# Optimization experiments

Measured on AMD Instinct MI355X. Metric: run time of the kernel, lower is better.

Reference implementation:

```python
import jax, jax.numpy as jnp
import numpy as np

N = 8192        # nodes
E = 131072      # template edges (avg degree 16)
IN_DIM = 2
H = 128         # hidden_dim
Z = 128         # z_dim
MAX_DEPTH = 32
DEPTH_PERTURB = 2
NEG = -1e30


def setup_inputs() -> dict:
    key = jax.random.key(0)
    ks = jax.random.split(key, 24)
    s = 0.05
    # template node features: col0 = node type in {0,1,2}, col1 = placeholder
    types = jax.random.randint(ks[0], (N,), 0, 3)
    x = jnp.stack([types.astype(jnp.float32),
                   jax.random.normal(ks[1], (N,))], axis=1)
    edge_index = jax.random.randint(ks[2], (2, E), 0, N)
    node_depth = jnp.sort(jax.random.randint(ks[3], (N,), 0, MAX_DEPTH))
    z = jax.random.normal(ks[4], (Z,))
    return {
        "x": x, "z": z,
        "edge_index": edge_index, "node_depth": node_depth,
        # GCNConv 1 & 2 (PyG style: y = x @ W^T, symmetric-normalized agg, + bias)
        "conv1_w": jax.random.normal(ks[5], (H, IN_DIM)) * s,
        "conv1_b": jnp.zeros((H,)),
        "conv2_w": jax.random.normal(ks[6], (H, H)) * s,
        "conv2_b": jnp.zeros((H,)),
        # node_proj: Linear(H+Z,H) -> ReLU -> Linear(H,H)
        "np1_w": jax.random.normal(ks[7], (H, H + Z)) * s,
        "np1_b": jnp.zeros((H,)),
        "np2_w": jax.random.normal(ks[8], (H, H)) * s,
        "np2_b": jnp.zeros((H,)),
        # src/tgt projections (bias-free)
        "src_w": jax.random.normal(ks[9], (H, H)) * s,
        "tgt_w": jax.random.normal(ks[10], (H, H)) * s,
        # inv_mlp: Linear(2H+Z,H) -> ReLU -> Linear(H,1)
        "inv1_w": jax.random.normal(ks[11], (H, 2 * H + Z)) * s,
        "inv1_b": jnp.zeros((H,)),
        "inv2_w": jax.random.normal(ks[12], (1, H)) * s,
        "inv2_b": jnp.zeros((1,)),
    }


def _gcn_conv(x, src, dst, W, b, n):
    # PyG GCNConv with self loops: out_i = sum_j norm_ij * (x_j W^T) + b
    xw = x @ W.T                                             # [n, out]
    deg = jax.ops.segment_sum(jnp.ones(src.shape, xw.dtype), dst,
                              num_segments=n) + 1.0          # self-loop
    rsq = jax.lax.rsqrt(deg)
    msg = (rsq[src] * rsq[dst])[:, None] * xw[src]           # [E, out]
    agg = jax.ops.segment_sum(msg, dst, num_segments=n)
    agg = agg + xw / deg[:, None]                            # self-loop term
    return agg + b


def reference(x, z, edge_index, node_depth,
              conv1_w, conv1_b, conv2_w, conv2_b,
              np1_w, np1_b, np2_w, np2_b,
              src_w, tgt_w, inv1_w, inv1_b, inv2_w, inv2_b):
    n = x.shape[0]
    types = x[:, 0].astype(jnp.int32)
    src, dst = edge_index[0], edge_index[1]

    # --- GCN encode ---
    h = jax.nn.relu(_gcn_conv(x, src, dst, conv1_w, conv1_b, n))
    h = jax.nn.relu(_gcn_conv(h, src, dst, conv2_w, conv2_b, n))

    # --- node_proj with broadcast z ---
    hz = jnp.concatenate([h, jnp.broadcast_to(z[None, :], (n, Z))], axis=1)
    h = jax.nn.relu(hz @ np1_w.T + np1_b) @ np2_w.T + np2_b  # [n, H]

    # --- vectorized per-target candidate attention scores ---
    Ht = h @ tgt_w.T                                         # [n, H]
    Hs = h @ src_w.T                                         # [n, H]
    scores = Ht @ Hs.T                                       # [n, n]: S[v,u]
    depth = node_depth
    # candidate u valid for target v iff depth[u] <= depth[v]-1+perturb
    cand_mask = depth[None, :] <= (depth[:, None] - 1 + DEPTH_PERTURB)
    scores_m = jnp.where(cand_mask, scores, NEG)
    top_vals, top_idx = jax.lax.top_k(scores_m, 2)           # [n,2] each

    num_cand = cand_mask.sum(axis=1)
    target_valid = (depth >= 1) & (types != 0)
    # type==2 (AND) gets k=2 fanins, other non-PI types k=1
    valid = jnp.stack([target_valid & (num_cand >= 1),
                       target_valid & (types == 2) & (num_cand >= 2)], axis=1)

    # --- per-edge inversion-bit MLP (vectorized over [n, 2] chosen edges) ---
    h_u = h[top_idx]                                         # [n,2,H]
    h_v = jnp.broadcast_to(h[:, None, :], (n, 2, H))
    z_b = jnp.broadcast_to(z[None, None, :], (n, 2, Z))
    inv_in = jnp.concatenate([h_u, h_v, z_b], axis=-1)       # [n,2,2H+Z]
    inv_logit = (jax.nn.relu(inv_in @ inv1_w.T + inv1_b) @ inv2_w.T + inv2_b)[..., 0]
    inv_bit = (jax.nn.sigmoid(inv_logit) > 0.5).astype(jnp.int32)

    return top_vals, inv_logit, top_idx, inv_bit, valid
```

## Files before the change

### kernel.cpp

```cpp
#include <hip/hip_runtime.h>

#define NN 8192
#define EE 131072
#define HH 128
#define NEGV -1.0e30f
#define SEG 128
#define NSEG (NN / SEG)
#define VT 128

typedef __attribute__((ext_vector_type(8))) short bf16x8;
typedef __attribute__((ext_vector_type(4))) float f32x4;

__device__ __forceinline__ unsigned short f2bf(float f) {
    unsigned int u = __float_as_uint(f);
    unsigned int r = u + 0x7fffu + ((u >> 16) & 1u);
    return (unsigned short)(r >> 16);
}
__device__ __forceinline__ float bf2f(unsigned short b) {
    return __uint_as_float((unsigned int)b << 16);
}


__global__ __launch_bounds__(256) void k_deg(const int* __restrict__ dst, int* __restrict__ degi) {
    int t = blockIdx.x * 256 + threadIdx.x;
    if (t < EE) atomicAdd(&degi[dst[t]], 1);
}

__global__ __launch_bounds__(1024) void k_scan(const int* __restrict__ degi, int* __restrict__ rowptr,
                                               float* __restrict__ dinv, float* __restrict__ rsq) {
    __shared__ int ls[1024];
    int tid = threadIdx.x;
    int base = tid * 8;
    int loc[8]; int s = 0;
#pragma unroll
    for (int i = 0; i < 8; i++) {
        int dg = degi[base + i];
        loc[i] = s; s += dg;
        double d = (double)(dg + 1);
        dinv[base + i] = (float)(1.0 / d);
        rsq[base + i] = (float)(1.0 / sqrt(d));
    }
    ls[tid] = s; __syncthreads();
    int tot = s;
    for (int d = 1; d < 1024; d <<= 1) {
        int v = (tid >= d) ? ls[tid - d] : 0;
        __syncthreads();
        ls[tid] += v;
        __syncthreads();
    }
    int pre = ls[tid] - tot;
#pragma unroll
    for (int i = 0; i < 8; i++) rowptr[base + i] = pre + loc[i];
    if (tid == 1023) rowptr[NN] = pre + tot;
}

__global__ __launch_bounds__(256) void k_fill(const int* __restrict__ src, const int* __restrict__ dst,
                                              const int* __restrict__ rowptr, int* __restrict__ cursor,
                                              int* __restrict__ ecsr) {
    int t = blockIdx.x * 256 + threadIdx.x;
    if (t < EE) {
        int d = dst[t];
        int pos = atomicAdd(&cursor[d], 1);
        ecsr[rowptr[d] + pos] = src[t];
    }
}


__global__ __launch_bounds__(256) void k_gather1(const int* __restrict__ rowptr, const int* __restrict__ ecsr,
                                                 const float* __restrict__ rsq, const float* __restrict__ dinv,
                                                 const float* __restrict__ x, const float* __restrict__ w,
                                                 const float* __restrict__ bias, float* __restrict__ out) {
    int g = blockIdx.x * 256 + threadIdx.x;
    int d = g >> 6, lane = g & 63;
    if (d >= NN) return;
    float w0a = w[lane * 2], w1a = w[lane * 2 + 1];
    float w0b = w[(lane + 64) * 2], w1b = w[(lane + 64) * 2 + 1];
    int s0 = rowptr[d], s1 = rowptr[d + 1];
    float rd = rsq[d];
    float a0 = 0.f, a1 = 0.f;
    for (int sl = s0; sl < s1; sl++) {
        int s = ecsr[sl];
        float x0 = x[s * 2], x1 = x[s * 2 + 1];
        float f = rsq[s] * rd;
        a0 = fmaf(f, x0 * w0a + x1 * w1a, a0);
        a1 = fmaf(f, x0 * w0b + x1 * w1b, a1);
    }
    float x0d = x[d * 2], x1d = x[d * 2 + 1], di = dinv[d];
    a0 = fmaf(x0d * w0a + x1d * w1a, di, a0) + bias[lane];
    a1 = fmaf(x0d * w0b + x1d * w1b, di, a1) + bias[64 + lane];
    out[d * HH + lane] = fmaxf(a0, 0.f);
    out[d * HH + 64 + lane] = fmaxf(a1, 0.f);
}


__global__ __launch_bounds__(256) void k_gather2(const int* __restrict__ rowptr, const int* __restrict__ ecsr,
                                                 const float* __restrict__ rsq, const float* __restrict__ dinv,
                                                 const float* __restrict__ xw, const float* __restrict__ bias,
                                                 float* __restrict__ out) {
    int g = blockIdx.x * 256 + threadIdx.x;
    int d = g >> 6, lane = g & 63;
    if (d >= NN) return;
    int s0 = rowptr[d], s1 = rowptr[d + 1];
    float rd = rsq[d];
    float a0 = 0.f, a1 = 0.f;
    for (int sl = s0; sl < s1; sl++) {
        int s = ecsr[sl];
        float f = rsq[s] * rd;
        a0 = fmaf(f, xw[s * HH + lane], a0);
        a1 = fmaf(f, xw[s * HH + 64 + lane], a1);
    }
    float di = dinv[d];
    a0 = fmaf(xw[d * HH + lane], di, a0) + bias[lane];
    a1 = fmaf(xw[d * HH + 64 + lane], di, a1) + bias[64 + lane];
    out[d * HH + lane] = fmaxf(a0, 0.f);
    out[d * HH + 64 + lane] = fmaxf(a1, 0.f);
}


__global__ __launch_bounds__(256) void k_prep(const float* __restrict__ conv2_w, const float* __restrict__ np1_w,
                                              const float* __restrict__ np2_w, const float* __restrict__ src_w,
                                              const float* __restrict__ tgt_w, const float* __restrict__ inv1_w,
                                              const float* __restrict__ np1_b, const float* __restrict__ inv1_b,
                                              const float* __restrict__ z, float* __restrict__ T,
                                              float* __restrict__ c1, float* __restrict__ cz) {
    int y = blockIdx.y;
    if (y < 7) {
        int t = blockIdx.x * 256 + threadIdx.x;
        int j = t >> 7, k = t & 127;
        const float* W; int stride, off;
        switch (y) {
            case 0:  W = conv2_w; stride = 128; off = 0;   break;
            case 1:  W = np1_w;   stride = 256; off = 0;   break;
            case 2:  W = np2_w;   stride = 128; off = 0;   break;
            case 3:  W = src_w;   stride = 128; off = 0;   break;
            case 4:  W = tgt_w;   stride = 128; off = 0;   break;
            case 5:  W = inv1_w;  stride = 384; off = 0;   break;
            default: W = inv1_w;  stride = 384; off = 128; break;
        }
        T[y * 16384 + k * 128 + j] = W[j * stride + off + k];
    } else if (blockIdx.x == 0) {
        int tid = threadIdx.x;
        if (tid < 128) {
            float s = np1_b[tid];
            for (int k = 0; k < 128; k++) s += z[k] * np1_w[tid * 256 + 128 + k];
            c1[tid] = s;
        } else {
            int j = tid - 128;
            float s = inv1_b[j];
            for (int k = 0; k < 128; k++) s += z[k] * inv1_w[j * 384 + 256 + k];
            cz[j] = s;
        }
    }
}


__global__ __launch_bounds__(256) void k_gemm128(const float* __restrict__ A, const float* __restrict__ WT,
                                                 const float* __restrict__ bias, float* __restrict__ out,
                                                 int relu) {
    __shared__ float As[32][33];
    __shared__ float Bs[32][128];
    int tid = threadIdx.x;
    int tx = tid & 31, ty = tid >> 5;
    int row0 = blockIdx.x * 32;
    float acc[4][4] = {};
    for (int k0 = 0; k0 < 128; k0 += 32) {
        {
            int r = tid >> 3, k = (tid & 7) << 2;
            float4 v = *(const float4*)&A[(row0 + r) * HH + k0 + k];
            As[r][k] = v.x; As[r][k + 1] = v.y; As[r][k + 2] = v.z; As[r][k + 3] = v.w;
        }
#pragma unroll
        for (int i = 0; i < 4; i++) {
            int kk = (tid >> 5) + i * 8;
            int c = (tid & 31) << 2;
            *(float4*)&Bs[kk][c] = *(const float4*)&WT[(k0 + kk) * HH + c];
        }
        __syncthreads();
#pragma unroll 8
        for (int kk = 0; kk < 32; kk++) {
            float a0 = As[ty * 4 + 0][kk], a1 = As[ty * 4 + 1][kk];
            float a2 = As[ty * 4 + 2][kk], a3 = As[ty * 4 + 3][kk];
            float4 b = *(const float4*)&Bs[kk][tx * 4];
            acc[0][0] = fmaf(a0, b.x, acc[0][0]); acc[0][1] = fmaf(a0, b.y, acc[0][1]);
            acc[0][2] = fmaf(a0, b.z, acc[0][2]); acc[0][3] = fmaf(a0, b.w, acc[0][3]);
            acc[1][0] = fmaf(a1, b.x, acc[1][0]); acc[1][1] = fmaf(a1, b.y, acc[1][1]);
            acc[1][2] = fmaf(a1, b.z, acc[1][2]); acc[1][3] = fmaf(a1, b.w, acc[1][3]);
            acc[2][0] = fmaf(a2, b.x, acc[2][0]); acc[2][1] = fmaf(a2, b.y, acc[2][1]);
            acc[2][2] = fmaf(a2, b.z, acc[2][2]); acc[2][3] = fmaf(a2, b.w, acc[2][3]);
            acc[3][0] = fmaf(a3, b.x, acc[3][0]); acc[3][1] = fmaf(a3, b.y, acc[3][1]);
            acc[3][2] = fmaf(a3, b.z, acc[3][2]); acc[3][3] = fmaf(a3, b.w, acc[3][3]);
        }
        __syncthreads();
    }
#pragma unroll
    for (int i = 0; i < 4; i++) {
        float4 v = make_float4(acc[i][0], acc[i][1], acc[i][2], acc[i][3]);
        if (bias) {
            v.x += bias[tx * 4]; v.y += bias[tx * 4 + 1];
            v.z += bias[tx * 4 + 2]; v.w += bias[tx * 4 + 3];
        }
        if (relu) {
            v.x = fmaxf(v.x, 0.f); v.y = fmaxf(v.y, 0.f);
            v.z = fmaxf(v.z, 0.f); v.w = fmaxf(v.w, 0.f);
        }
        *(float4*)&out[(row0 + ty * 4 + i) * HH + tx * 4] = v;
    }
}


__global__ __launch_bounds__(256) void k_mlp(const float* __restrict__ h2g, const float* __restrict__ T,
                                             const float* __restrict__ c1, const float* __restrict__ np2_b,
                                             float* __restrict__ h3g,
                                             unsigned short* __restrict__ HtP, unsigned short* __restrict__ HsP) {
    __shared__ float bufA[32][132];
    __shared__ float bufB[32][132];
    __shared__ float Bs[32][128];
    int tid = threadIdx.x;
    int tx = tid & 31, ty = tid >> 5;
    int row0 = blockIdx.x * 32;
#pragma unroll
    for (int p = 0; p < 4; p++) {
        int q = p * 256 + tid;
        int r = q >> 5, c4 = (q & 31) * 4;
        *(float4*)&bufA[r][c4] = *(const float4*)&h2g[(size_t)(row0 + r) * HH + c4];
    }
    __syncthreads();
    for (int g = 0; g < 4; g++) {
        const float* WT;
        switch (g) {
            case 0:  WT = T + 1 * 16384; break;
            case 1:  WT = T + 2 * 16384; break;
            case 2:  WT = T + 4 * 16384; break;
            default: WT = T + 3 * 16384; break;
        }
        float (*src)[132] = (g == 1) ? bufB : bufA;
        float acc[4][4] = {};
        for (int k0 = 0; k0 < 128; k0 += 32) {
#pragma unroll
            for (int i = 0; i < 4; i++) {
                int kk = (tid >> 5) + i * 8;
                int c = (tid & 31) << 2;
                *(float4*)&Bs[kk][c] = *(const float4*)&WT[(k0 + kk) * HH + c];
            }
            __syncthreads();
#pragma unroll 8
            for (int kk = 0; kk < 32; kk++) {
                float a0 = src[ty * 4 + 0][k0 + kk], a1 = src[ty * 4 + 1][k0 + kk];
                float a2 = src[ty * 4 + 2][k0 + kk], a3 = src[ty * 4 + 3][k0 + kk];
                float4 b = *(const float4*)&Bs[kk][tx * 4];
                acc[0][0] = fmaf(a0, b.x, acc[0][0]); acc[0][1] = fmaf(a0, b.y, acc[0][1]);
                acc[0][2] = fmaf(a0, b.z, acc[0][2]); acc[0][3] = fmaf(a0, b.w, acc[0][3]);
                acc[1][0] = fmaf(a1, b.x, acc[1][0]); acc[1][1] = fmaf(a1, b.y, acc[1][1]);
                acc[1][2] = fmaf(a1, b.z, acc[1][2]); acc[1][3] = fmaf(a1, b.w, acc[1][3]);
                acc[2][0] = fmaf(a2, b.x, acc[2][0]); acc[2][1] = fmaf(a2, b.y, acc[2][1]);
                acc[2][2] = fmaf(a2, b.z, acc[2][2]); acc[2][3] = fmaf(a2, b.w, acc[2][3]);
                acc[3][0] = fmaf(a3, b.x, acc[3][0]); acc[3][1] = fmaf(a3, b.y, acc[3][1]);
                acc[3][2] = fmaf(a3, b.z, acc[3][2]); acc[3][3] = fmaf(a3, b.w, acc[3][3]);
            }
            __syncthreads();
        }
        if (g == 0) {
#pragma unroll
            for (int i = 0; i < 4; i++)
#pragma unroll
                for (int jj = 0; jj < 4; jj++)
                    bufB[ty * 4 + i][tx * 4 + jj] = fmaxf(acc[i][jj] + c1[tx * 4 + jj], 0.f);
        } else if (g == 1) {
#pragma unroll
            for (int i = 0; i < 4; i++) {
                float4 v;
                v.x = acc[i][0] + np2_b[tx * 4 + 0];
                v.y = acc[i][1] + np2_b[tx * 4 + 1];
                v.z = acc[i][2] + np2_b[tx * 4 + 2];
                v.w = acc[i][3] + np2_b[tx * 4 + 3];
                bufA[ty * 4 + i][tx * 4 + 0] = v.x; bufA[ty * 4 + i][tx * 4 + 1] = v.y;
                bufA[ty * 4 + i][tx * 4 + 2] = v.z; bufA[ty * 4 + i][tx * 4 + 3] = v.w;
                *(float4*)&h3g[(size_t)(row0 + ty * 4 + i) * HH + tx * 4] = v;
            }
        } else {
            unsigned short* PP = (g == 2) ? HtP : HsP;
            int chunk = tx >> 3;
            int cic = (tx * 4) & 31;
#pragma unroll
            for (int i = 0; i < 4; i++) {
                int row = row0 + ty * 4 + i;
                size_t off = (size_t)row * 384 + chunk * 96 + cic;
                unsigned short h[4], m[4], lo[4];
#pragma unroll
                for (int jj = 0; jj < 4; jj++) {
                    float val = acc[i][jj];
                    unsigned short hb = f2bf(val);
                    float r1 = val - bf2f(hb);
                    unsigned short mb = f2bf(r1);
                    float r2 = r1 - bf2f(mb);
                    h[jj] = hb; m[jj] = mb; lo[jj] = f2bf(r2);
                }
                *(uint2*)&PP[off] = make_uint2((unsigned)h[0] | ((unsigned)h[1] << 16),
                                               (unsigned)h[2] | ((unsigned)h[3] << 16));
                *(uint2*)&PP[off + 32] = make_uint2((unsigned)m[0] | ((unsigned)m[1] << 16),
                                                    (unsigned)m[2] | ((unsigned)m[3] << 16));
                *(uint2*)&PP[off + 64] = make_uint2((unsigned)lo[0] | ((unsigned)lo[1] << 16),
                                                    (unsigned)lo[2] | ((unsigned)lo[3] << 16));
            }
        }
    }
}


__global__ __launch_bounds__(256) void k_cnt_valid(const int* __restrict__ depth, const float* __restrict__ x,
                                                   int* __restrict__ cnt, float* __restrict__ out) {
    int v = blockIdx.x * 256 + threadIdx.x;
    if (v >= NN) return;
    int limit = depth[v] + 1;
    int lo = 0, hi = NN;
    while (lo < hi) { int mid = (lo + hi) >> 1; if (depth[mid] <= limit) lo = mid + 1; else hi = mid; }
    cnt[v] = lo;
    int type = (int)(x[v * 2] + 0.5f);
    bool tv = (depth[v] >= 1) && (type != 0);
    out[4 * NN * 2 + v * 2 + 0] = (tv && lo >= 1) ? 1.0f : 0.0f;
    out[4 * NN * 2 + v * 2 + 1] = (tv && type == 2 && lo >= 2) ? 1.0f : 0.0f;
}


__global__ __launch_bounds__(64) void k_tiles(const int* __restrict__ cnt, int* __restrict__ nact,
                                              int* __restrict__ tlist, int* __restrict__ ntiles) {
    int lane = threadIdx.x;
    int cmax = cnt[lane * VT + VT - 1];
    int n = (cmax + SEG - 1) / SEG;
    nact[lane] = n;
    int x = n;
    for (int off = 1; off < 64; off <<= 1) {
        int y = __shfl_up(x, off, 64);
        if (lane >= off) x += y;
    }
    int base = x - n;
    for (int s = 0; s < n; s++) tlist[base + s] = (lane << 8) | s;
    if (lane == 63) *ntiles = x;
}


__global__ __launch_bounds__(256, 2) void k_top2_stage1(
    const unsigned short* __restrict__ HtP, const unsigned short* __restrict__ HsP,
    const int* __restrict__ cnt, const int* __restrict__ tlist,
    const int* __restrict__ ntiles, int* __restrict__ tctr,
    float* __restrict__ pval, int* __restrict__ pidx) {
    __shared__ unsigned short Bsh[64 * 392];
    __shared__ int tsh;
    int tid = threadIdx.x;
    int wave = tid >> 6, lane = tid & 63;
    int l = lane & 15, quad = lane >> 4;
    int nt = *ntiles;
    for (;;) {
        __syncthreads();
        if (tid == 0) tsh = atomicAdd(tctr, 1);
        __syncthreads();
        int t = tsh;
        if (t >= nt) return;
        int code = tlist[t];
        int v0 = (code >> 8) * VT;
        int seg = code & 255;
        int ub0 = seg * SEG;
        int vbase = v0 + wave * 32;
        bf16x8 afr[2][4][3];
#pragma unroll
        for (int s = 0; s < 2; s++) {
            const unsigned short* ap = &HtP[(size_t)(vbase + s * 16 + l) * 384 + quad * 8];
#pragma unroll
            for (int c = 0; c < 4; c++) {
                afr[s][c][0] = *(const bf16x8*)&ap[c * 96];
                afr[s][c][1] = *(const bf16x8*)&ap[c * 96 + 32];
                afr[s][c][2] = *(const bf16x8*)&ap[c * 96 + 64];
            }
        }
        int creg[8];
#pragma unroll
        for (int i = 0; i < 8; i++)
            creg[i] = cnt[vbase + (i >> 2) * 16 + quad * 4 + (i & 3)];
        float t1v[8], t2v[8]; int t1i[8], t2i[8];
#pragma unroll
        for (int i = 0; i < 8; i++) { t1v[i] = NEGV; t2v[i] = NEGV; t1i[i] = 0x7fffffff; t2i[i] = 0x7fffffff; }
        int cmax = cnt[v0 + VT - 1];
        int uend = ub0 + SEG; if (uend > cmax) uend = cmax;
        for (int cb = ub0; cb < uend; cb += 64) {
            __syncthreads();
#pragma unroll
            for (int gi = 0; gi < 12; gi++) {
                int g = gi * 256 + tid;
                int r = g / 48, w = g - r * 48;
                *(uint4*)&Bsh[r * 392 + w * 8] = *(const uint4*)&HsP[(size_t)(cb + r) * 384 + w * 8];
            }
            __syncthreads();
            int cend = cb + 64; if (cend > uend) cend = uend;
            for (int u0 = cb; u0 < cend; u0 += 16) {
                int u = u0 + l;
                const unsigned short* bp = &Bsh[(u0 - cb + l) * 392 + quad * 8];
                f32x4 acc0 = {0.f, 0.f, 0.f, 0.f}, acc1 = {0.f, 0.f, 0.f, 0.f};
#pragma unroll
                for (int c = 0; c < 4; c++) {
                    bf16x8 bh = *(const bf16x8*)&bp[c * 96];
                    bf16x8 bm = *(const bf16x8*)&bp[c * 96 + 32];
                    bf16x8 bl = *(const bf16x8*)&bp[c * 96 + 64];
                    acc0 = __builtin_amdgcn_mfma_f32_16x16x32_bf16(afr[0][c][0], bh, acc0, 0, 0, 0);
                    acc1 = __builtin_amdgcn_mfma_f32_16x16x32_bf16(afr[1][c][0], bh, acc1, 0, 0, 0);
                    acc0 = __builtin_amdgcn_mfma_f32_16x16x32_bf16(afr[0][c][0], bm, acc0, 0, 0, 0);
                    acc1 = __builtin_amdgcn_mfma_f32_16x16x32_bf16(afr[1][c][0], bm, acc1, 0, 0, 0);
                    acc0 = __builtin_amdgcn_mfma_f32_16x16x32_bf16(afr[0][c][1], bh, acc0, 0, 0, 0);
                    acc1 = __builtin_amdgcn_mfma_f32_16x16x32_bf16(afr[1][c][1], bh, acc1, 0, 0, 0);
                    acc0 = __builtin_amdgcn_mfma_f32_16x16x32_bf16(afr[0][c][0], bl, acc0, 0, 0, 0);
                    acc1 = __builtin_amdgcn_mfma_f32_16x16x32_bf16(afr[1][c][0], bl, acc1, 0, 0, 0);
                    acc0 = __builtin_amdgcn_mfma_f32_16x16x32_bf16(afr[0][c][2], bh, acc0, 0, 0, 0);
                    acc1 = __builtin_amdgcn_mfma_f32_16x16x32_bf16(afr[1][c][2], bh, acc1, 0, 0, 0);
                    acc0 = __builtin_amdgcn_mfma_f32_16x16x32_bf16(afr[0][c][1], bm, acc0, 0, 0, 0);
                    acc1 = __builtin_amdgcn_mfma_f32_16x16x32_bf16(afr[1][c][1], bm, acc1, 0, 0, 0);
                }
#pragma unroll
                for (int i = 0; i < 8; i++) {
                    float sv = (i < 4) ? acc0[i & 3] : acc1[i & 3];
                    float val = (u < creg[i]) ? sv : NEGV;
                    if (val > t1v[i] || (val == t1v[i] && u < t1i[i])) {
                        t2v[i] = t1v[i]; t2i[i] = t1i[i]; t1v[i] = val; t1i[i] = u;
                    } else if (val > t2v[i] || (val == t2v[i] && u < t2i[i])) {
                        t2v[i] = val; t2i[i] = u;
                    }
                }
            }
        }
#pragma unroll
        for (int m = 1; m <= 8; m <<= 1) {
#pragma unroll
            for (int i = 0; i < 8; i++) {
                float ov1 = __shfl_xor(t1v[i], m, 64);
                int   oi1 = __shfl_xor(t1i[i], m, 64);
                float ov2 = __shfl_xor(t2v[i], m, 64);
                int   oi2 = __shfl_xor(t2i[i], m, 64);
                bool b1 = (ov1 > t1v[i]) || (ov1 == t1v[i] && oi1 < t1i[i]);
                float w1v = b1 ? ov1 : t1v[i]; int w1i = b1 ? oi1 : t1i[i];
                float l1v = b1 ? t1v[i] : ov1; int l1i = b1 ? t1i[i] : oi1;
                float c2v = b1 ? ov2 : t2v[i]; int c2i = b1 ? oi2 : t2i[i];
                bool b2 = (l1v > c2v) || (l1v == c2v && l1i < c2i);
                t1v[i] = w1v; t1i[i] = w1i;
                t2v[i] = b2 ? l1v : c2v; t2i[i] = b2 ? l1i : c2i;
            }
        }
        if (l == 0) {
#pragma unroll
            for (int i = 0; i < 8; i++) {
                int v = vbase + (i >> 2) * 16 + quad * 4 + (i & 3);
                int o = (v * NSEG + seg) * 2;
                pval[o] = t1v[i];     pidx[o] = t1i[i];
                pval[o + 1] = t2v[i]; pidx[o + 1] = t2i[i];
            }
        }
    }
}


__global__ __launch_bounds__(256) void k_merge_inv(const float* __restrict__ pval, const int* __restrict__ pidx,
                                                   const int* __restrict__ nact,
                                                   const float* __restrict__ P, const float* __restrict__ Q,
                                                   const float* __restrict__ cz, const float* __restrict__ w2,
                                                   const float* __restrict__ b2, float* __restrict__ out) {
    int gid = blockIdx.x * 256 + threadIdx.x;
    int v = gid >> 6, lane = gid & 63;
    if (v >= NN) return;
    int na = nact[v >> 7];
    float v1 = NEGV, v2 = NEGV; int i1 = 0x7fffffff, i2 = 0x7fffffff;
    if (lane < na) {
        int o = (v * NSEG + lane) * 2;
        v1 = pval[o];     i1 = pidx[o];
        v2 = pval[o + 1]; i2 = pidx[o + 1];
    }
#pragma unroll
    for (int m = 1; m <= 32; m <<= 1) {
        float ov1 = __shfl_xor(v1, m, 64);
        int   oi1 = __shfl_xor(i1, m, 64);
        float ov2 = __shfl_xor(v2, m, 64);
        int   oi2 = __shfl_xor(i2, m, 64);
        bool b1 = (ov1 > v1) || (ov1 == v1 && oi1 < i1);
        float w1v = b1 ? ov1 : v1; int w1i = b1 ? oi1 : i1;
        float l1v = b1 ? v1 : ov1; int l1i = b1 ? i1 : oi1;
        float c2v = b1 ? ov2 : v2; int c2i = b1 ? oi2 : i2;
        bool b2 = (l1v > c2v) || (l1v == c2v && l1i < c2i);
        v1 = w1v; i1 = w1i;
        v2 = b2 ? l1v : c2v; i2 = b2 ? l1i : c2i;
    }
    if (na == 0) { v1 = NEGV; v2 = NEGV; i1 = 0; i2 = 1; }
    int u1 = i1, u2 = i2;
    float cza = cz[lane], czb = cz[64 + lane];
    float w2a = w2[lane], w2b = w2[64 + lane];
    float Qa = Q[(size_t)v * HH + lane], Qb = Q[(size_t)v * HH + 64 + lane];
    float p0 = fmaxf(P[(size_t)u1 * HH + lane] + Qa + cza, 0.f) * w2a +
               fmaxf(P[(size_t)u1 * HH + 64 + lane] + Qb + czb, 0.f) * w2b;
    float p1 = fmaxf(P[(size_t)u2 * HH + lane] + Qa + cza, 0.f) * w2a +
               fmaxf(P[(size_t)u2 * HH + 64 + lane] + Qb + czb, 0.f) * w2b;
#pragma unroll
    for (int off = 32; off >= 1; off >>= 1) {
        p0 += __shfl_down(p0, off, 64);
        p1 += __shfl_down(p1, off, 64);
    }
    if (lane == 0) {
        float bb = b2[0];
        float l0 = p0 + bb, l1 = p1 + bb;
        out[v * 2 + 0] = v1; out[v * 2 + 1] = v2;
        out[NN * 2 + v * 2 + 0] = l0;
        out[NN * 2 + v * 2 + 1] = l1;
        out[2 * NN * 2 + v * 2 + 0] = (float)i1;
        out[2 * NN * 2 + v * 2 + 1] = (float)i2;
        out[3 * NN * 2 + v * 2 + 0] = (l0 > 0.f) ? 1.f : 0.f;
        out[3 * NN * 2 + v * 2 + 1] = (l1 > 0.f) ? 1.f : 0.f;
    }
}


extern "C" void kernel_launch(void* const* d_in, const int* in_sizes, int n_in,
                              void* d_out, int out_size, void* d_ws, size_t ws_size,
                              hipStream_t stream) {
    const float* x       = (const float*)d_in[0];
    const float* z       = (const float*)d_in[1];
    const int*   eidx    = (const int*)d_in[2];
    const int*   depth   = (const int*)d_in[3];
    const float* conv1_w = (const float*)d_in[4];
    const float* conv1_b = (const float*)d_in[5];
    const float* conv2_w = (const float*)d_in[6];
    const float* conv2_b = (const float*)d_in[7];
    const float* np1_w   = (const float*)d_in[8];
    const float* np1_b   = (const float*)d_in[9];
    const float* np2_w   = (const float*)d_in[10];
    const float* np2_b   = (const float*)d_in[11];
    const float* src_w   = (const float*)d_in[12];
    const float* tgt_w   = (const float*)d_in[13];
    const float* inv1_w  = (const float*)d_in[14];
    const float* inv1_b  = (const float*)d_in[15];
    const float* inv2_w  = (const float*)d_in[16];
    const float* inv2_b  = (const float*)d_in[17];
    float* out = (float*)d_out;
    float* wsf = (float*)d_ws;

    const int NH = NN * HH;
    float* R0 = wsf;
    float* R1 = wsf + (size_t)NH;
    unsigned short* HtP = (unsigned short*)R1;
    unsigned short* HsP = HtP + 3 * (size_t)NH;
    float* P = wsf + (size_t)NH;
    float* Q = wsf + 2 * (size_t)NH;
    float* pval = wsf + 4 * (size_t)NH;
    int*   pidx = (int*)(wsf + 5 * (size_t)NH);
    float* T  = wsf + 6 * (size_t)NH;
    float* c1 = T + 7 * 16384;
    float* cz = c1 + 128;
    float* rsq  = cz + 128;
    float* dinv = rsq + NN;
    int* degi   = (int*)(dinv + NN);
    int* rowptr = degi + NN;
    int* cursor = rowptr + NN + 1;
    int* cnt    = cursor + NN;
    int* nact   = cnt + NN;
    int* ntiles = nact + 64;
    int* tctr   = ntiles + 1;
    int* tlist  = tctr + 1;
    int* ecsr   = tlist + 4096;

    const int* esrc = eidx;
    const int* edst = eidx + EE;

    hipMemsetAsync(degi, 0, NN * sizeof(int), stream);
    hipMemsetAsync(cursor, 0, NN * sizeof(int), stream);
    hipMemsetAsync(tctr, 0, sizeof(int), stream);
    k_prep<<<dim3(64, 8), 256, 0, stream>>>(conv2_w, np1_w, np2_w, src_w, tgt_w, inv1_w,
                                            np1_b, inv1_b, z, T, c1, cz);
    k_deg<<<EE / 256, 256, 0, stream>>>(edst, degi);
    k_scan<<<1, 1024, 0, stream>>>(degi, rowptr, dinv, rsq);
    k_fill<<<EE / 256, 256, 0, stream>>>(esrc, edst, rowptr, cursor, ecsr);
    k_gather1<<<NN * 64 / 256, 256, 0, stream>>>(rowptr, ecsr, rsq, dinv, x, conv1_w, conv1_b, R0);
    k_gemm128<<<256, 256, 0, stream>>>(R0, T + 0 * 16384, nullptr, R1, 0);
    k_gather2<<<NN * 64 / 256, 256, 0, stream>>>(rowptr, ecsr, rsq, dinv, R1, conv2_b, R0);
    k_mlp<<<256, 256, 0, stream>>>(R0, T, c1, np2_b, R0, HtP, HsP);
    k_cnt_valid<<<NN / 256, 256, 0, stream>>>(depth, x, cnt, out);
    k_tiles<<<1, 64, 0, stream>>>(cnt, nact, tlist, ntiles);
    k_top2_stage1<<<768, 256, 0, stream>>>(HtP, HsP, cnt, tlist, ntiles, tctr, pval, pidx);
    k_gemm128<<<256, 256, 0, stream>>>(R0, T + 5 * 16384, nullptr, P, 0);
    k_gemm128<<<256, 256, 0, stream>>>(R0, T + 6 * 16384, nullptr, Q, 0);
    k_merge_inv<<<NN / 4, 256, 0, stream>>>(pval, pidx, nact, P, Q, cz, inv2_w, inv2_b, out);
}
```

Baseline: 332.2 us.

## Fuse cnt/tile kernels, merge P/Q GEMMs, swizzle LDS and prefetch B fragments

Result: slower. 385.3 us (+16.0%).

```diff
diff --git a/kernel.cpp b/kernel.cpp
--- a/kernel.cpp
+++ b/kernel.cpp
@@ -207,6 +207,52 @@
     }
 }
 
+__global__ __launch_bounds__(256) void k_gemmPQ(const float* __restrict__ A, const float* __restrict__ T,
+                                                float* __restrict__ P, float* __restrict__ Q) {
+    __shared__ float As[32][33];
+    __shared__ float Bs[32][128];
+    const float* WT = (blockIdx.y == 0) ? (T + 5 * 16384) : (T + 6 * 16384);
+    float* outp = (blockIdx.y == 0) ? P : Q;
+    int tid = threadIdx.x;
+    int tx = tid & 31, ty = tid >> 5;
+    int row0 = blockIdx.x * 32;
+    float acc[4][4] = {};
+    for (int k0 = 0; k0 < 128; k0 += 32) {
+        {
+            int r = tid >> 3, k = (tid & 7) << 2;
+            float4 v = *(const float4*)&A[(row0 + r) * HH + k0 + k];
+            As[r][k] = v.x; As[r][k + 1] = v.y; As[r][k + 2] = v.z; As[r][k + 3] = v.w;
+        }
+#pragma unroll
+        for (int i = 0; i < 4; i++) {
+            int kk = (tid >> 5) + i * 8;
+            int c = (tid & 31) << 2;
+            *(float4*)&Bs[kk][c] = *(const float4*)&WT[(k0 + kk) * HH + c];
+        }
+        __syncthreads();
+#pragma unroll 8
+        for (int kk = 0; kk < 32; kk++) {
+            float a0 = As[ty * 4 + 0][kk], a1 = As[ty * 4 + 1][kk];
+            float a2 = As[ty * 4 + 2][kk], a3 = As[ty * 4 + 3][kk];
+            float4 b = *(const float4*)&Bs[kk][tx * 4];
+            acc[0][0] = fmaf(a0, b.x, acc[0][0]); acc[0][1] = fmaf(a0, b.y, acc[0][1]);
+            acc[0][2] = fmaf(a0, b.z, acc[0][2]); acc[0][3] = fmaf(a0, b.w, acc[0][3]);
+            acc[1][0] = fmaf(a1, b.x, acc[1][0]); acc[1][1] = fmaf(a1, b.y, acc[1][1]);
+            acc[1][2] = fmaf(a1, b.z, acc[1][2]); acc[1][3] = fmaf(a1, b.w, acc[1][3]);
+            acc[2][0] = fmaf(a2, b.x, acc[2][0]); acc[2][1] = fmaf(a2, b.y, acc[2][1]);
+            acc[2][2] = fmaf(a2, b.z, acc[2][2]); acc[2][3] = fmaf(a2, b.w, acc[2][3]);
+            acc[3][0] = fmaf(a3, b.x, acc[3][0]); acc[3][1] = fmaf(a3, b.y, acc[3][1]);
+            acc[3][2] = fmaf(a3, b.z, acc[3][2]); acc[3][3] = fmaf(a3, b.w, acc[3][3]);
+        }
+        __syncthreads();
+    }
+#pragma unroll
+    for (int i = 0; i < 4; i++) {
+        float4 v = make_float4(acc[i][0], acc[i][1], acc[i][2], acc[i][3]);
+        *(float4*)&outp[(row0 + ty * 4 + i) * HH + tx * 4] = v;
+    }
+}
+
 
 __global__ __launch_bounds__(256) void k_mlp(const float* __restrict__ h2g, const float* __restrict__ T,
                                              const float* __restrict__ c1, const float* __restrict__ np2_b,
@@ -307,48 +353,53 @@
 }
 
 
-__global__ __launch_bounds__(256) void k_cnt_valid(const int* __restrict__ depth, const float* __restrict__ x,
-                                                   int* __restrict__ cnt, float* __restrict__ out) {
-    int v = blockIdx.x * 256 + threadIdx.x;
-    if (v >= NN) return;
-    int limit = depth[v] + 1;
-    int lo = 0, hi = NN;
-    while (lo < hi) { int mid = (lo + hi) >> 1; if (depth[mid] <= limit) lo = mid + 1; else hi = mid; }
-    cnt[v] = lo;
-    int type = (int)(x[v * 2] + 0.5f);
-    bool tv = (depth[v] >= 1) && (type != 0);
-    out[4 * NN * 2 + v * 2 + 0] = (tv && lo >= 1) ? 1.0f : 0.0f;
-    out[4 * NN * 2 + v * 2 + 1] = (tv && type == 2 && lo >= 2) ? 1.0f : 0.0f;
-}
-
-
-__global__ __launch_bounds__(64) void k_tiles(const int* __restrict__ cnt, int* __restrict__ nact,
-                                              int* __restrict__ tlist, int* __restrict__ ntiles) {
-    int lane = threadIdx.x;
-    int cmax = cnt[lane * VT + VT - 1];
-    int n = (cmax + SEG - 1) / SEG;
-    nact[lane] = n;
-    int x = n;
-    for (int off = 1; off < 64; off <<= 1) {
-        int y = __shfl_up(x, off, 64);
-        if (lane >= off) x += y;
-    }
-    int base = x - n;
-    for (int s = 0; s < n; s++) tlist[base + s] = (lane << 8) | s;
-    if (lane == 63) *ntiles = x;
-}
-
-
-__global__ __launch_bounds__(256, 2) void k_top2_stage1(
+__global__ __launch_bounds__(1024) void k_cnt_tiles(const int* __restrict__ depth, const float* __restrict__ x,
+                                                    int* __restrict__ cnt, int* __restrict__ nact,
+                                                    int* __restrict__ tlist, int* __restrict__ ntiles,
+                                                    float* __restrict__ out) {
+    __shared__ int ls[64];
+    int tid = threadIdx.x;
+#pragma unroll
+    for (int i = 0; i < 8; i++) {
+        int v = tid * 8 + i;
+        int limit = depth[v] + 1;
+        int lo = 0, hi = NN;
+        while (lo < hi) { int mid = (lo + hi) >> 1; if (depth[mid] <= limit) lo = mid + 1; else hi = mid; }
+        cnt[v] = lo;
+        int type = (int)(x[v * 2] + 0.5f);
+        bool tv = (depth[v] >= 1) && (type != 0);
+        out[4 * NN * 2 + v * 2 + 0] = (tv && lo >= 1) ? 1.0f : 0.0f;
+        out[4 * NN * 2 + v * 2 + 1] = (tv && type == 2 && lo >= 2) ? 1.0f : 0.0f;
+        if ((v & (VT - 1)) == VT - 1) ls[v >> 7] = lo;
+    }
+    __syncthreads();
+    if (tid < 64) {
+        int cmax = ls[tid];
+        int n = (cmax + SEG - 1) / SEG;
+        nact[tid] = n;
+        int xp = n;
+        for (int off = 1; off < 64; off <<= 1) {
+            int y = __shfl_up(xp, off, 64);
+            if (tid >= off) xp += y;
+        }
+        int base = xp - n;
+        for (int s = 0; s < n; s++) tlist[base + s] = (tid << 8) | s;
+        if (tid == 63) *ntiles = xp;
+    }
+}
+
+
+__global__ __launch_bounds__(256, 3) void k_top2_stage1(
     const unsigned short* __restrict__ HtP, const unsigned short* __restrict__ HsP,
     const int* __restrict__ cnt, const int* __restrict__ tlist,
     const int* __restrict__ ntiles, int* __restrict__ tctr,
     float* __restrict__ pval, int* __restrict__ pidx) {
-    __shared__ unsigned short Bsh[64 * 392];
+    __shared__ unsigned short Bsh[64 * 384];
     __shared__ int tsh;
     int tid = threadIdx.x;
     int wave = tid >> 6, lane = tid & 63;
     int l = lane & 15, quad = lane >> 4;
+    int xr = l & 7;
     int nt = *ntiles;
     for (;;) {
         __syncthreads();
@@ -387,19 +438,21 @@
             for (int gi = 0; gi < 12; gi++) {
                 int g = gi * 256 + tid;
                 int r = g / 48, w = g - r * 48;
-                *(uint4*)&Bsh[r * 392 + w * 8] = *(const uint4*)&HsP[(size_t)(cb + r) * 384 + w * 8];
+                int phys = w ^ (r & 7);
+                *(uint4*)&Bsh[r * 384 + phys * 8] = *(const uint4*)&HsP[(size_t)(cb + r) * 384 + w * 8];
             }
             __syncthreads();
             int cend = cb + 64; if (cend > uend) cend = uend;
             for (int u0 = cb; u0 < cend; u0 += 16) {
                 int u = u0 + l;
-                const unsigned short* bp = &Bsh[(u0 - cb + l) * 392 + quad * 8];
+                int rowb = (u0 - cb + l) * 384;
                 f32x4 acc0 = {0.f, 0.f, 0.f, 0.f}, acc1 = {0.f, 0.f, 0.f, 0.f};
+#define BLD(c, p) (*(const bf16x8*)&Bsh[rowb + (((c) * 12 + (p) * 4 + quad) ^ xr) * 8])
+                bf16x8 bh = BLD(0, 0), bm = BLD(0, 1), bl = BLD(0, 2);
 #pragma unroll
                 for (int c = 0; c < 4; c++) {
-                    bf16x8 bh = *(const bf16x8*)&bp[c * 96];
-                    bf16x8 bm = *(const bf16x8*)&bp[c * 96 + 32];
-                    bf16x8 bl = *(const bf16x8*)&bp[c * 96 + 64];
+                    bf16x8 nh, nm, nl;
+                    if (c < 3) { nh = BLD(c + 1, 0); nm = BLD(c + 1, 1); nl = BLD(c + 1, 2); }
                     acc0 = __builtin_amdgcn_mfma_f32_16x16x32_bf16(afr[0][c][0], bh, acc0, 0, 0, 0);
                     acc1 = __builtin_amdgcn_mfma_f32_16x16x32_bf16(afr[1][c][0], bh, acc1, 0, 0, 0);
                     acc0 = __builtin_amdgcn_mfma_f32_16x16x32_bf16(afr[0][c][0], bm, acc0, 0, 0, 0);
@@ -412,7 +465,9 @@
                     acc1 = __builtin_amdgcn_mfma_f32_16x16x32_bf16(afr[1][c][2], bh, acc1, 0, 0, 0);
                     acc0 = __builtin_amdgcn_mfma_f32_16x16x32_bf16(afr[0][c][1], bm, acc0, 0, 0, 0);
                     acc1 = __builtin_amdgcn_mfma_f32_16x16x32_bf16(afr[1][c][1], bm, acc1, 0, 0, 0);
+                    if (c < 3) { bh = nh; bm = nm; bl = nl; }
                 }
+#undef BLD
 #pragma unroll
                 for (int i = 0; i < 8; i++) {
                     float sv = (i < 4) ? acc0[i & 3] : acc1[i & 3];
@@ -575,10 +630,8 @@
     k_gemm128<<<256, 256, 0, stream>>>(R0, T + 0 * 16384, nullptr, R1, 0);
     k_gather2<<<NN * 64 / 256, 256, 0, stream>>>(rowptr, ecsr, rsq, dinv, R1, conv2_b, R0);
     k_mlp<<<256, 256, 0, stream>>>(R0, T, c1, np2_b, R0, HtP, HsP);
-    k_cnt_valid<<<NN / 256, 256, 0, stream>>>(depth, x, cnt, out);
-    k_tiles<<<1, 64, 0, stream>>>(cnt, nact, tlist, ntiles);
+    k_cnt_tiles<<<1, 1024, 0, stream>>>(depth, x, cnt, nact, tlist, ntiles, out);
     k_top2_stage1<<<768, 256, 0, stream>>>(HtP, HsP, cnt, tlist, ntiles, tctr, pval, pidx);
-    k_gemm128<<<256, 256, 0, stream>>>(R0, T + 5 * 16384, nullptr, P, 0);
-    k_gemm128<<<256, 256, 0, stream>>>(R0, T + 6 * 16384, nullptr, Q, 0);
+    k_gemmPQ<<<dim3(256, 2), 256, 0, stream>>>(R0, T, P, Q);
     k_merge_inv<<<NN / 4, 256, 0, stream>>>(pval, pidx, nact, P, Q, cz, inv2_w, inv2_b, out);
 }
```
